# Optimization experiments

Measured on AMD Instinct MI355X. Metric: run time of the kernel, lower is better.

The kernel has to match this reference:

```python
import jax, jax.numpy as jnp
import numpy as np

D_MODEL = 1024
N_HEADS = 16

def setup_inputs() -> dict:
    key = jax.random.key(0)
    ks = jax.random.split(key, 11)
    B, L, S, D = 2, 2048, 2048, D_MODEL
    s = 1.0 / np.sqrt(D)
    return {
        "Q": jax.random.normal(ks[0], (B, L, D), jnp.float32),
        "K": jax.random.normal(ks[1], (B, S, D), jnp.float32),
        "V": jax.random.normal(ks[2], (B, S, D), jnp.float32),
        "Wq": jax.random.normal(ks[3], (D, D), jnp.float32) * s,
        "bq": jnp.zeros((D,), jnp.float32),
        "Wk": jax.random.normal(ks[4], (D, D), jnp.float32) * s,
        "bk": jnp.zeros((D,), jnp.float32),
        "Wv": jax.random.normal(ks[5], (D, D), jnp.float32) * s,
        "bv": jnp.zeros((D,), jnp.float32),
        "We": jax.random.normal(ks[6], (D, D), jnp.float32) * s,
        "be": jnp.zeros((D,), jnp.float32),
    }

def reference(Q, K, V, Wq, bq, Wk, bk, Wv, bv, We, be):
    B, L, D = Q.shape
    S = K.shape[1]
    H = N_HEADS
    E = D // H
    # projections, split heads
    q = (Q @ Wq + bq).reshape(B, L, H, E)
    k = (K @ Wk + bk).reshape(B, S, H, E)
    v = (V @ Wv + bv).reshape(B, S, H, E)
    scale = 1.0 / np.sqrt(E)
    scores = jnp.einsum('blhe,bshe->bhls', q, k)  # [B,H,L,S]
    A = jax.nn.softmax(scale * scores, axis=-1)   # dropout is identity in eval
    out = jnp.einsum('bhls,bshd->blhd', A, v).reshape(B, L, H * E)
    return out @ We + be
```

## Files before the change

### kernel.cpp

```cpp
#include <hip/hip_runtime.h>
#include <hip/hip_bf16.h>
#include <stdint.h>

typedef __bf16 bf16_t;
typedef bf16_t bf16x8 __attribute__((ext_vector_type(8)));
typedef float  f32x4  __attribute__((ext_vector_type(4)));
typedef float  f32x16 __attribute__((ext_vector_type(16)));

#define GLOAD16(gp, lp) __builtin_amdgcn_global_load_lds( \
    (const __attribute__((address_space(1))) void*)(gp),  \
    (__attribute__((address_space(3))) void*)(lp), 16, 0, 0)

#define EXP2F(x) __builtin_amdgcn_exp2f(x)

__device__ inline uint32_t pack2(float lo, float hi) {
    union { bf16_t h[2]; uint32_t u; } x;
    x.h[0] = (bf16_t)lo; x.h[1] = (bf16_t)hi;
    return x.u;
}

__global__ __launch_bounds__(256) void wtrans_kernel(
    const float* __restrict__ Wq, const float* __restrict__ Wk,
    const float* __restrict__ Wv, const float* __restrict__ We,
    bf16_t* __restrict__ WqT, bf16_t* __restrict__ WkT,
    bf16_t* __restrict__ WvT, bf16_t* __restrict__ WeT)
{
    __shared__ bf16_t T[64][65];
    const float* W = (blockIdx.z == 0) ? Wq : (blockIdx.z == 1) ? Wk
                   : (blockIdx.z == 2) ? Wv : We;
    bf16_t* O = (blockIdx.z == 0) ? WqT : (blockIdx.z == 1) ? WkT
              : (blockIdx.z == 2) ? WvT : WeT;
    const int k0 = blockIdx.y * 64, n0 = blockIdx.x * 64;
    const int t = threadIdx.x;
    for (int i = 0; i < 16; ++i) {
        int flat = t + i * 256;
        int r = flat >> 6, c = flat & 63;
        T[r][c] = (bf16_t)W[(size_t)(k0 + r) * 1024 + n0 + c];
    }
    __syncthreads();
    for (int i = 0; i < 16; ++i) {
        int flat = t + i * 256;
        int n = flat >> 6, kk = flat & 63;
        O[(size_t)(n0 + n) * 1024 + k0 + kk] = T[kk][n];
    }
}

__global__ __launch_bounds__(256)
void cvt_kernel(const float* __restrict__ X0, const float* __restrict__ X1,
                const float* __restrict__ X2,
                bf16_t* __restrict__ Y0, bf16_t* __restrict__ Y1,
                bf16_t* __restrict__ Y2)
{
    const float* X = (blockIdx.y == 0) ? X0 : (blockIdx.y == 1) ? X1 : X2;
    bf16_t*      Y = (blockIdx.y == 0) ? Y0 : (blockIdx.y == 1) ? Y1 : Y2;
    size_t i0 = ((size_t)blockIdx.x * 256 + threadIdx.x) * 8;
    float4 v0 = *(const float4*)(X + i0);
    float4 v1 = *(const float4*)(X + i0 + 4);
    bf16x8 pv;
    pv[0] = (bf16_t)v0.x; pv[1] = (bf16_t)v0.y;
    pv[2] = (bf16_t)v0.z; pv[3] = (bf16_t)v0.w;
    pv[4] = (bf16_t)v1.x; pv[5] = (bf16_t)v1.y;
    pv[6] = (bf16_t)v1.z; pv[7] = (bf16_t)v1.w;
    *(bf16x8*)(Y + i0) = pv;
}

template<bool BATCHED>
__global__ __launch_bounds__(256)
void gemm3_kernel(const bf16_t* __restrict__ A0, const bf16_t* __restrict__ A1,
                  const bf16_t* __restrict__ A2,
                  const bf16_t* __restrict__ B0, const bf16_t* __restrict__ B1,
                  const bf16_t* __restrict__ B2,
                  const float* __restrict__ b0, const float* __restrict__ b1,
                  const float* __restrict__ b2,
                  void* __restrict__ C0, void* __restrict__ C1,
                  void* __restrict__ C2)
{
    constexpr int M = 4096, K = 1024, N = 1024;
    __shared__ bf16_t As[128 * 64];
    __shared__ bf16_t Bs[128 * 64];

    const int msel = BATCHED ? blockIdx.y : 0;
    const bf16_t* Ab   = (msel == 0) ? A0 : (msel == 1) ? A1 : A2;
    const bf16_t* Bt   = (msel == 0) ? B0 : (msel == 1) ? B1 : B2;
    const float*  bias = (msel == 0) ? b0 : (msel == 1) ? b1 : b2;
    void*         Cv   = (msel == 0) ? C0 : (msel == 1) ? C1 : C2;
    const int omode = BATCHED ? ((msel == 2) ? 2 : 0) : 1;

    const int xcd = blockIdx.x & 7, idx = blockIdx.x >> 3;
    const int bm = (xcd << 2) | (idx >> 3), bn = idx & 7;
    const int row0 = bm * 128, col0 = bn * 128;
    const int t = threadIdx.x, w = t >> 6, l = t & 63;
    const int wr = w >> 1, wc = w & 1;

    f32x4 acc[4][4];
    #pragma unroll
    for (int i = 0; i < 4; ++i)
        #pragma unroll
        for (int j = 0; j < 4; ++j)
            #pragma unroll
            for (int c = 0; c < 4; ++c) acc[i][j][c] = 0.f;

    for (int k0 = 0; k0 < K; k0 += 64) {
        #pragma unroll
        for (int i = 0; i < 4; ++i) {
            int chunk = (w * 4 + i) * 64 + l;
            int r = chunk >> 3, c = chunk & 7;
            int soff = (c ^ (r & 7)) * 8;
            GLOAD16(Ab + (size_t)(row0 + r) * K + k0 + soff, &As[(w * 4 + i) * 512]);
            GLOAD16(Bt + (size_t)(col0 + r) * K + k0 + soff, &Bs[(w * 4 + i) * 512]);
        }
        __syncthreads();

        #pragma unroll
        for (int eks = 0; eks < 2; ++eks) {
            bf16x8 af[4], bfv[4];
            #pragma unroll
            for (int mi = 0; mi < 4; ++mi) {
                int row = wr * 64 + mi * 16 + (l & 15);
                int sl = (eks * 4 + (l >> 4)) ^ (row & 7);
                af[mi] = *(const bf16x8*)&As[row * 64 + sl * 8];
            }
            #pragma unroll
            for (int ni = 0; ni < 4; ++ni) {
                int row = wc * 64 + ni * 16 + (l & 15);
                int sl = (eks * 4 + (l >> 4)) ^ (row & 7);
                bfv[ni] = *(const bf16x8*)&Bs[row * 64 + sl * 8];
            }
            __builtin_amdgcn_s_setprio(1);
            #pragma unroll
            for (int mi = 0; mi < 4; ++mi)
                #pragma unroll
                for (int ni = 0; ni < 4; ++ni)
                    acc[mi][ni] = __builtin_amdgcn_mfma_f32_16x16x32_bf16(
                        af[mi], bfv[ni], acc[mi][ni], 0, 0, 0);
            __builtin_amdgcn_s_setprio(0);
        }
        __syncthreads();
    }

    #pragma unroll
    for (int mi = 0; mi < 4; ++mi)
        #pragma unroll
        for (int ni = 0; ni < 4; ++ni) {
            int col = col0 + wc * 64 + ni * 16 + (l & 15);
            float bv = bias[col];
            int rowb = row0 + wr * 64 + mi * 16 + (l >> 4) * 4;
            if (omode == 2) {
                union { bf16_t h[4]; uint64_t q; } pk;
                #pragma unroll
                for (int j = 0; j < 4; ++j)
                    pk.h[j] = (bf16_t)(acc[mi][ni][j] + bv);
                *(uint64_t*)((bf16_t*)Cv + (size_t)col * M + rowb) = pk.q;
            } else if (omode == 1) {
                #pragma unroll
                for (int j = 0; j < 4; ++j)
                    ((float*)Cv)[(size_t)(rowb + j) * N + col] = acc[mi][ni][j] + bv;
            } else {
                #pragma unroll
                for (int j = 0; j < 4; ++j)
                    ((bf16_t*)Cv)[(size_t)(rowb + j) * N + col] = (bf16_t)(acc[mi][ni][j] + bv);
            }
        }
}

__global__ __launch_bounds__(256)
void attn4_kernel(const bf16_t* __restrict__ qp, const bf16_t* __restrict__ kp,
                  const bf16_t* __restrict__ vT, bf16_t* __restrict__ o)
{
    __shared__ bf16_t Ks[2][4096];
    __shared__ bf16_t Vs[2][4096];
    const int qb = blockIdx.x, bh = blockIdx.y;
    const int b = bh >> 4, h = bh & 15;
    const int t = threadIdx.x, w = t >> 6, l = t & 63;
    const int ql = l & 31, hh = l >> 5;
    const float M0 = 8.0f * 1.44269504f;

    const bf16_t* kbase = kp + ((size_t)b * 2048) * 1024 + h * 64;
    const bf16_t* vbase = vT + ((size_t)h * 64) * 4096 + (size_t)b * 2048;
    const int q0 = qb * 128 + w * 32;

    bf16x8 qf[4];
    {
        const bf16_t* qrow = qp + ((size_t)b * 2048 + q0 + ql) * 1024 + h * 64;
        const float qs = 0.125f * 1.44269504f;
        #pragma unroll
        for (int eks = 0; eks < 4; ++eks) {
            bf16x8 v = *(const bf16x8*)(qrow + eks * 16 + hh * 8);
            #pragma unroll
            for (int j = 0; j < 8; ++j) v[j] = (bf16_t)((float)v[j] * qs);
            qf[eks] = v;
        }
    }

    f32x16 acc0, acc1;
    #pragma unroll
    for (int r = 0; r < 16; ++r) { acc0[r] = 0.f; acc1[r] = 0.f; }
    float lsum = 0.f;

    const int r0 = t >> 3, r1 = 32 + (t >> 3), g = t & 7;
    const int w0off = r0 * 64 + ((g ^ (r0 & 7)) * 8);
    const int w1off = r1 * 64 + ((g ^ (r1 & 7)) * 8);

    {
        bf16x8 a = *(const bf16x8*)(kbase + (size_t)r0 * 1024 + g * 8);
        bf16x8 c = *(const bf16x8*)(kbase + (size_t)r1 * 1024 + g * 8);
        bf16x8 d = *(const bf16x8*)(vbase + (size_t)r0 * 4096 + g * 8);
        bf16x8 e = *(const bf16x8*)(vbase + (size_t)r1 * 4096 + g * 8);
        *(bf16x8*)&Ks[0][w0off] = a;  *(bf16x8*)&Ks[0][w1off] = c;
        *(bf16x8*)&Vs[0][w0off] = d;  *(bf16x8*)&Vs[0][w1off] = e;
    }
    __syncthreads();

    int cur = 0;
    for (int tile = 0; tile < 32; ++tile) {
        bf16x8 kr0, kr1, vr0, vr1;
        const bool pf = (tile + 1 < 32);
        if (pf) {
            const int s1 = (tile + 1) * 64;
            kr0 = *(const bf16x8*)(kbase + (size_t)(s1 + r0) * 1024 + g * 8);
            kr1 = *(const bf16x8*)(kbase + (size_t)(s1 + r1) * 1024 + g * 8);
            vr0 = *(const bf16x8*)(vbase + (size_t)r0 * 4096 + s1 + g * 8);
            vr1 = *(const bf16x8*)(vbase + (size_t)r1 * 4096 + s1 + g * 8);
        }

        f32x16 sA, sB;
        #pragma unroll
        for (int r = 0; r < 16; ++r) { sA[r] = 0.f; sB[r] = 0.f; }
        __builtin_amdgcn_s_setprio(1);
        #pragma unroll
        for (int eks = 0; eks < 4; ++eks) {
            bf16x8 k0 = *(const bf16x8*)&Ks[cur][ql * 64 + (((2 * eks + hh) ^ (ql & 7)) * 8)];
            bf16x8 k1 = *(const bf16x8*)&Ks[cur][(32 + ql) * 64 + (((2 * eks + hh) ^ (ql & 7)) * 8)];
            sA = __builtin_amdgcn_mfma_f32_32x32x16_bf16(k0, qf[eks], sA, 0, 0, 0);
            sB = __builtin_amdgcn_mfma_f32_32x32x16_bf16(k1, qf[eks], sB, 0, 0, 0);
        }
        __builtin_amdgcn_s_setprio(0);

        uint32_t wA[8], wB[8];
        float rs = 0.f;
        #pragma unroll
        for (int i = 0; i < 8; ++i) {
            float p0 = EXP2F(sA[2 * i]     - M0);
            float p1 = EXP2F(sA[2 * i + 1] - M0);
            rs += p0 + p1;  wA[i] = pack2(p0, p1);
            float p2 = EXP2F(sB[2 * i]     - M0);
            float p3 = EXP2F(sB[2 * i + 1] - M0);
            rs += p2 + p3;  wB[i] = pack2(p2, p3);
        }
        rs += __shfl_xor(rs, 32);
        lsum += rs;

        #pragma unroll
        for (int ks = 0; ks < 4; ++ks) {
            const int base = (ks & 1) * 4;
            uint32_t a0 = (ks < 2) ? wA[base]     : wB[base];
            uint32_t a1 = (ks < 2) ? wA[base + 1] : wB[base + 1];
            uint32_t a2 = (ks < 2) ? wA[base + 2] : wB[base + 2];
            uint32_t a3 = (ks < 2) ? wA[base + 3] : wB[base + 3];
            uint32_t x0 = (uint32_t)__shfl_xor((int)a0, 32);
            uint32_t x1 = (uint32_t)__shfl_xor((int)a1, 32);
            uint32_t x2 = (uint32_t)__shfl_xor((int)a2, 32);
            uint32_t x3 = (uint32_t)__shfl_xor((int)a3, 32);
            union { uint32_t u[4]; bf16x8 v; } pb;
            pb.u[0] = hh ? x2 : a0;
            pb.u[1] = hh ? x3 : a1;
            pb.u[2] = hh ? a2 : x0;
            pb.u[3] = hh ? a3 : x1;
            bf16x8 v0 = *(const bf16x8*)&Vs[cur][ql * 64 + (((2 * ks + hh) ^ (ql & 7)) * 8)];
            bf16x8 v1 = *(const bf16x8*)&Vs[cur][(32 + ql) * 64 + (((2 * ks + hh) ^ (ql & 7)) * 8)];
            __builtin_amdgcn_s_setprio(1);
            acc0 = __builtin_amdgcn_mfma_f32_32x32x16_bf16(v0, pb.v, acc0, 0, 0, 0);
            acc1 = __builtin_amdgcn_mfma_f32_32x32x16_bf16(v1, pb.v, acc1, 0, 0, 0);
            __builtin_amdgcn_s_setprio(0);
        }

        if (pf) {
            *(bf16x8*)&Ks[cur ^ 1][w0off] = kr0;
            *(bf16x8*)&Ks[cur ^ 1][w1off] = kr1;
            *(bf16x8*)&Vs[cur ^ 1][w0off] = vr0;
            *(bf16x8*)&Vs[cur ^ 1][w1off] = vr1;
        }
        __syncthreads();
        cur ^= 1;
    }

    bf16_t* sc = &Ks[0][0];
    const float inv = 1.0f / lsum;
    #pragma unroll
    for (int r = 0; r < 16; ++r) {
        int e = (r & 3) + 8 * (r >> 2) + 4 * hh;
        sc[w * 2048 + ql * 64 + (((e >> 3) ^ (ql & 7)) * 8) + (e & 7)] =
            (bf16_t)(acc0[r] * inv);
        int e2 = e + 32;
        sc[w * 2048 + ql * 64 + (((e2 >> 3) ^ (ql & 7)) * 8) + (e2 & 7)] =
            (bf16_t)(acc1[r] * inv);
    }
    __syncthreads();
    #pragma unroll
    for (int it = 0; it < 4; ++it) {
        int ci = it * 64 + l;
        int qr = ci >> 3, ec = ci & 7;
        bf16x8 ov = *(const bf16x8*)&sc[w * 2048 + qr * 64 + ((ec ^ (qr & 7)) * 8)];
        *(bf16x8*)(o + ((size_t)b * 2048 + q0 + qr) * 1024 + h * 64 + ec * 8) = ov;
    }
}

extern "C" void kernel_launch(void* const* d_in, const int* in_sizes, int n_in,
                              void* d_out, int out_size, void* d_ws, size_t ws_size,
                              hipStream_t stream)
{
    const float* Q  = (const float*)d_in[0];
    const float* K  = (const float*)d_in[1];
    const float* V  = (const float*)d_in[2];
    const float* Wq = (const float*)d_in[3];
    const float* bq = (const float*)d_in[4];
    const float* Wk = (const float*)d_in[5];
    const float* bk = (const float*)d_in[6];
    const float* Wv = (const float*)d_in[7];
    const float* bv = (const float*)d_in[8];
    const float* We = (const float*)d_in[9];
    const float* be = (const float*)d_in[10];
    float* out = (float*)d_out;

    bf16_t* ws = (bf16_t*)d_ws;
    bf16_t* WqT = ws;
    bf16_t* WkT = WqT + 1024 * 1024;
    bf16_t* WvT = WkT + 1024 * 1024;
    bf16_t* WeT = WvT + 1024 * 1024;
    bf16_t* qp  = WeT + 1024 * 1024;
    bf16_t* kp  = qp  + 4096 * 1024;
    bf16_t* vt  = kp  + 4096 * 1024;
    bf16_t* ao  = vt  + 4096 * 1024;
    bf16_t* Qb  = ao  + 4096 * 1024;
    bf16_t* Kb  = Qb  + 4096 * 1024;
    bf16_t* Vb  = Kb  + 4096 * 1024;

    dim3 blk(256);

    hipLaunchKernelGGL(wtrans_kernel, dim3(16, 16, 4), blk, 0, stream,
                       Wq, Wk, Wv, We, WqT, WkT, WvT, WeT);

    hipLaunchKernelGGL(cvt_kernel, dim3(2048, 3), blk, 0, stream,
                       Q, K, V, Qb, Kb, Vb);

    hipLaunchKernelGGL((gemm3_kernel<true>), dim3(256, 3), blk, 0, stream,
                       Qb, Kb, Vb, WqT, WkT, WvT, bq, bk, bv,
                       (void*)qp, (void*)kp, (void*)vt);

    hipLaunchKernelGGL(attn4_kernel, dim3(16, 32), blk, 0, stream,
                       qp, kp, vt, ao);

    hipLaunchKernelGGL((gemm3_kernel<false>), dim3(256, 1), blk, 0, stream,
                       ao, (const bf16_t*)nullptr, (const bf16_t*)nullptr,
                       WeT, (const bf16_t*)nullptr, (const bf16_t*)nullptr,
                       be, (const float*)nullptr, (const float*)nullptr,
                       (void*)out, (void*)nullptr, (void*)nullptr);
}
```

Baseline: 141.1 us.

## Load attention K/V tiles directly to LDS and remap blocks per XCD

Register-staged K/V prefetch in the attention kernel is replaced by global_load_lds direct-to-shared copies, with the XOR swizzle moved to the global-side addresses. This frees VGPRs and removes the LDS store phase. The grid is flattened to 1D and remapped so blocks of the same (batch, head) group land on the same XCD, improving L2 reuse of K/V. The fixed max offset is folded into the MFMA accumulator init, which saves a subtract per score.

```diff
diff --git a/kernel.cpp b/kernel.cpp
--- a/kernel.cpp
+++ b/kernel.cpp
@@ -164,12 +164,15 @@
 }
 
 __global__ __launch_bounds__(256)
-void attn4_kernel(const bf16_t* __restrict__ qp, const bf16_t* __restrict__ kp,
+void attn6_kernel(const bf16_t* __restrict__ qp, const bf16_t* __restrict__ kp,
                   const bf16_t* __restrict__ vT, bf16_t* __restrict__ o)
 {
     __shared__ bf16_t Ks[2][4096];
     __shared__ bf16_t Vs[2][4096];
-    const int qb = blockIdx.x, bh = blockIdx.y;
+    const int bid = blockIdx.x;
+    const int xcd = bid & 7, j = bid >> 3;
+    const int bh = (xcd << 2) | (j & 3);
+    const int qb = j >> 2;
     const int b = bh >> 4, h = bh & 15;
     const int t = threadIdx.x, w = t >> 6, l = t & 63;
     const int ql = l & 31, hh = l >> 5;
@@ -187,7 +190,7 @@
         for (int eks = 0; eks < 4; ++eks) {
             bf16x8 v = *(const bf16x8*)(qrow + eks * 16 + hh * 8);
             #pragma unroll
-            for (int j = 0; j < 8; ++j) v[j] = (bf16_t)((float)v[j] * qs);
+            for (int jj = 0; jj < 8; ++jj) v[jj] = (bf16_t)((float)v[jj] * qs);
             qf[eks] = v;
         }
     }
@@ -197,35 +200,29 @@
     for (int r = 0; r < 16; ++r) { acc0[r] = 0.f; acc1[r] = 0.f; }
     float lsum = 0.f;
 
-    const int r0 = t >> 3, r1 = 32 + (t >> 3), g = t & 7;
-    const int w0off = r0 * 64 + ((g ^ (r0 & 7)) * 8);
-    const int w1off = r1 * 64 + ((g ^ (r1 & 7)) * 8);
-
-    {
-        bf16x8 a = *(const bf16x8*)(kbase + (size_t)r0 * 1024 + g * 8);
-        bf16x8 c = *(const bf16x8*)(kbase + (size_t)r1 * 1024 + g * 8);
-        bf16x8 d = *(const bf16x8*)(vbase + (size_t)r0 * 4096 + g * 8);
-        bf16x8 e = *(const bf16x8*)(vbase + (size_t)r1 * 4096 + g * 8);
-        *(bf16x8*)&Ks[0][w0off] = a;  *(bf16x8*)&Ks[0][w1off] = c;
-        *(bf16x8*)&Vs[0][w0off] = d;  *(bf16x8*)&Vs[0][w1off] = e;
-    }
+    const int ci0 = (w * 2) * 64 + l, ci1 = (w * 2 + 1) * 64 + l;
+    const int gr0 = ci0 >> 3, gc0 = ci0 & 7, so0 = ((gc0 ^ (gr0 & 7)) * 8);
+    const int gr1 = ci1 >> 3, gc1 = ci1 & 7, so1 = ((gc1 ^ (gr1 & 7)) * 8);
+
+    GLOAD16(kbase + (size_t)gr0 * 1024 + so0, &Ks[0][(w * 2) * 512]);
+    GLOAD16(kbase + (size_t)gr1 * 1024 + so1, &Ks[0][(w * 2 + 1) * 512]);
+    GLOAD16(vbase + (size_t)gr0 * 4096 + so0, &Vs[0][(w * 2) * 512]);
+    GLOAD16(vbase + (size_t)gr1 * 4096 + so1, &Vs[0][(w * 2 + 1) * 512]);
     __syncthreads();
 
     int cur = 0;
     for (int tile = 0; tile < 32; ++tile) {
-        bf16x8 kr0, kr1, vr0, vr1;
-        const bool pf = (tile + 1 < 32);
-        if (pf) {
+        if (tile + 1 < 32) {
             const int s1 = (tile + 1) * 64;
-            kr0 = *(const bf16x8*)(kbase + (size_t)(s1 + r0) * 1024 + g * 8);
-            kr1 = *(const bf16x8*)(kbase + (size_t)(s1 + r1) * 1024 + g * 8);
-            vr0 = *(const bf16x8*)(vbase + (size_t)r0 * 4096 + s1 + g * 8);
-            vr1 = *(const bf16x8*)(vbase + (size_t)r1 * 4096 + s1 + g * 8);
+            GLOAD16(kbase + (size_t)(s1 + gr0) * 1024 + so0, &Ks[cur ^ 1][(w * 2) * 512]);
+            GLOAD16(kbase + (size_t)(s1 + gr1) * 1024 + so1, &Ks[cur ^ 1][(w * 2 + 1) * 512]);
+            GLOAD16(vbase + (size_t)gr0 * 4096 + s1 + so0, &Vs[cur ^ 1][(w * 2) * 512]);
+            GLOAD16(vbase + (size_t)gr1 * 4096 + s1 + so1, &Vs[cur ^ 1][(w * 2 + 1) * 512]);
         }
 
         f32x16 sA, sB;
         #pragma unroll
-        for (int r = 0; r < 16; ++r) { sA[r] = 0.f; sB[r] = 0.f; }
+        for (int r = 0; r < 16; ++r) { sA[r] = -M0; sB[r] = -M0; }
         __builtin_amdgcn_s_setprio(1);
         #pragma unroll
         for (int eks = 0; eks < 4; ++eks) {
@@ -240,11 +237,11 @@
         float rs = 0.f;
         #pragma unroll
         for (int i = 0; i < 8; ++i) {
-            float p0 = EXP2F(sA[2 * i]     - M0);
-            float p1 = EXP2F(sA[2 * i + 1] - M0);
+            float p0 = EXP2F(sA[2 * i]);
+            float p1 = EXP2F(sA[2 * i + 1]);
             rs += p0 + p1;  wA[i] = pack2(p0, p1);
-            float p2 = EXP2F(sB[2 * i]     - M0);
-            float p3 = EXP2F(sB[2 * i + 1] - M0);
+            float p2 = EXP2F(sB[2 * i]);
+            float p3 = EXP2F(sB[2 * i + 1]);
             rs += p2 + p3;  wB[i] = pack2(p2, p3);
         }
         rs += __shfl_xor(rs, 32);
@@ -274,12 +271,6 @@
             __builtin_amdgcn_s_setprio(0);
         }
 
-        if (pf) {
-            *(bf16x8*)&Ks[cur ^ 1][w0off] = kr0;
-            *(bf16x8*)&Ks[cur ^ 1][w1off] = kr1;
-            *(bf16x8*)&Vs[cur ^ 1][w0off] = vr0;
-            *(bf16x8*)&Vs[cur ^ 1][w1off] = vr1;
-        }
         __syncthreads();
         cur ^= 1;
     }
@@ -347,7 +338,7 @@
                        Qb, Kb, Vb, WqT, WkT, WvT, bq, bk, bv,
                        (void*)qp, (void*)kp, (void*)vt);
 
-    hipLaunchKernelGGL(attn4_kernel, dim3(16, 32), blk, 0, stream,
+    hipLaunchKernelGGL(attn6_kernel, dim3(512), blk, 0, stream,
                        qp, kp, vt, ao);
 
     hipLaunchKernelGGL((gemm3_kernel<false>), dim3(256, 1), blk, 0, stream,
```

Result: faster. 138.0 us (-2.2%).
